# Kernel tuning notes

Hardware: AMD Instinct MI355X
Metric: run time of the kernel (lower is better)

The kernel has to match this reference:

```python
import jax, jax.numpy as jnp
import numpy as np

N = 100000   # nodes
E = 1600000  # edges
IN, H, C = 128, 128, 64
LN_EPS = 1e-5


def _xavier(key, fan_in, fan_out):
    lim = jnp.sqrt(6.0 / (fan_in + fan_out)).astype(jnp.float32)
    return jax.random.uniform(key, (fan_in, fan_out), jnp.float32, -lim, lim)


def setup_inputs() -> dict:
    key = jax.random.key(0)
    ks = jax.random.split(key, 6)
    feats = jax.random.normal(ks[0], (N, IN), jnp.float32)
    src = jax.random.randint(ks[1], (E,), 0, N, jnp.int32)
    dst = jax.random.randint(ks[2], (E,), 0, N, jnp.int32)
    return {
        "feats": feats, "src": src, "dst": dst,
        "W0": _xavier(ks[3], IN, H), "b0": jnp.zeros((H,), jnp.float32),
        "g0": jnp.ones((H,), jnp.float32), "be0": jnp.zeros((H,), jnp.float32),
        "W1": _xavier(ks[4], H, H), "b1": jnp.zeros((H,), jnp.float32),
        "g1": jnp.ones((H,), jnp.float32), "be1": jnp.zeros((H,), jnp.float32),
        "W2": _xavier(ks[5], H, C), "b2": jnp.zeros((C,), jnp.float32),
    }


def _gcn_agg(h, src, dst):
    # symmetric GCN normalization: out[v] = sum_{(u,v) in E} h[u] / sqrt(deg_out(u) * deg_in(v))
    ones = jnp.ones(src.shape, jnp.float32)
    deg_out = jax.ops.segment_sum(ones, src, num_segments=N)
    deg_in = jax.ops.segment_sum(ones, dst, num_segments=N)
    norm_o = jax.lax.rsqrt(jnp.maximum(deg_out, 1.0))
    norm_i = jax.lax.rsqrt(jnp.maximum(deg_in, 1.0))
    msg = (h * norm_o[:, None])[src]                       # [E, d] gather
    agg = jax.ops.segment_sum(msg, dst, num_segments=N)    # [N, d] scatter-add
    return agg * norm_i[:, None]


def _layernorm(x, gamma, beta):
    mu = jnp.mean(x, axis=-1, keepdims=True)
    var = jnp.mean(jnp.square(x - mu), axis=-1, keepdims=True)
    return (x - mu) * jax.lax.rsqrt(var + LN_EPS) * gamma + beta


def reference(feats, src, dst, W0, b0, g0, be0, W1, b1, g1, be1, W2, b2):
    # layer 0: agg -> matmul -> bias -> dropout(eval: identity) -> layernorm -> relu
    h = _gcn_agg(feats, src, dst) @ W0 + b0
    h = jax.nn.relu(_layernorm(h, g0, be0))
    # layer 1
    h = _gcn_agg(h, src, dst) @ W1 + b1
    h = jax.nn.relu(_layernorm(h, g1, be1))
    # final layer: agg -> matmul -> bias
    out = _gcn_agg(h, src, dst) @ W2 + b2
    return out
```

## Files before the change

### kernel.cpp

```cpp
#include <hip/hip_runtime.h>

constexpr float LN_EPS = 1e-5f;

typedef __bf16 bf16x8 __attribute__((ext_vector_type(8)));
typedef float f32x4 __attribute__((ext_vector_type(4)));

__device__ __forceinline__ unsigned short f2bf(float f) {
  unsigned int u = __float_as_uint(f);
  u = (u + 0x7fffu + ((u >> 16) & 1u)) >> 16;
  return (unsigned short)u;
}
__device__ __forceinline__ float bflo(unsigned int p) { return __uint_as_float(p << 16); }
__device__ __forceinline__ float bfhi(unsigned int p) { return __uint_as_float(p & 0xffff0000u); }

#define NPB 256
#define CHUNK 4096

__global__ __launch_bounds__(256) void passA_kernel(
    const int* __restrict__ src, const int* __restrict__ dst,
    int* __restrict__ cntD, int* __restrict__ cntS, int NB, int NBLK, int E) {
  extern __shared__ int sh[];
  for (int j = threadIdx.x; j < 2 * NB; j += 256) sh[j] = 0;
  __syncthreads();
  const int blk = blockIdx.x;
  const int base = blk * CHUNK;
  const int end = min(base + CHUNK, E);
  for (int i = base + threadIdx.x; i < end; i += 256) {
    atomicAdd(&sh[dst[i] >> 8], 1);
    atomicAdd(&sh[NB + (src[i] >> 8)], 1);
  }
  __syncthreads();
  for (int j = threadIdx.x; j < NB; j += 256) {
    cntD[j * NBLK + blk] = sh[j];
    cntS[j * NBLK + blk] = sh[NB + j];
  }
}

__global__ __launch_bounds__(512) void scan1_kernel(
    const int* __restrict__ cntD, const int* __restrict__ cntS,
    int* __restrict__ offLD, int* __restrict__ offLS,
    int* __restrict__ totD, int* __restrict__ totS, int NB, int NBLK) {
  __shared__ int p[512];
  const int t = threadIdx.x;
  const bool isS = blockIdx.x >= NB;
  const int b = isS ? blockIdx.x - NB : blockIdx.x;
  const int* cnt = isS ? cntS : cntD;
  int* offL = isS ? offLS : offLD;
  int own = (t < NBLK) ? cnt[b * NBLK + t] : 0;
  p[t] = own;
  __syncthreads();
  for (int off = 1; off < 512; off <<= 1) {
    int x = (t >= off) ? p[t - off] : 0;
    __syncthreads();
    p[t] += x;
    __syncthreads();
  }
  if (t < NBLK) offL[b * NBLK + t] = p[t] - own;
  if (t == 511) (isS ? totS : totD)[b] = p[511];
}

__global__ __launch_bounds__(512) void scan2_kernel(
    const int* __restrict__ totD, const int* __restrict__ totS,
    int* __restrict__ bktD, int* __restrict__ bktS,
    int* __restrict__ row_st, int NB, int N, int E) {
  __shared__ int p[512];
  const int t = threadIdx.x;
  int own = (t < NB) ? totD[t] : 0;
  p[t] = own;
  __syncthreads();
  for (int off = 1; off < 512; off <<= 1) {
    int x = (t >= off) ? p[t - off] : 0;
    __syncthreads();
    p[t] += x;
    __syncthreads();
  }
  if (t < NB) bktD[t] = p[t] - own;
  __syncthreads();
  int own2 = (t < NB) ? totS[t] : 0;
  p[t] = own2;
  __syncthreads();
  for (int off = 1; off < 512; off <<= 1) {
    int x = (t >= off) ? p[t - off] : 0;
    __syncthreads();
    p[t] += x;
    __syncthreads();
  }
  if (t < NB) bktS[t] = p[t] - own2;
  if (t == 0) {
    bktD[NB] = E;
    bktS[NB] = E;
    row_st[N] = E;
  }
}

__global__ __launch_bounds__(256) void passB_kernel(
    const int* __restrict__ src, const int* __restrict__ dst,
    const int* __restrict__ offLD, const int* __restrict__ offLS,
    const int* __restrict__ bkt_stD, const int* __restrict__ bkt_stS,
    unsigned int* __restrict__ packedD, unsigned char* __restrict__ srcS,
    int NB, int NBLK, int E) {
  __shared__ unsigned int sD[CHUNK];
  __shared__ unsigned short bD_[CHUNK];
  __shared__ unsigned char sS_[CHUNK];
  __shared__ unsigned short bS_[CHUNK];
  __shared__ int hD[512], lD[512], hS[512], lS[512];
  const int t = threadIdx.x;
  const int blk = blockIdx.x;
  const int base = blk * CHUNK;
  const int end = min(base + CHUNK, E);
  const int cnt = end - base;
  hD[t] = 0; hD[t + 256] = 0; hS[t] = 0; hS[t + 256] = 0;
  __syncthreads();
  for (int i = base + t; i < end; i += 256) {
    atomicAdd(&hD[dst[i] >> 8], 1);
    atomicAdd(&hS[src[i] >> 8], 1);
  }
  __syncthreads();
  int oD0 = hD[t], oD1 = hD[t + 256], oS0 = hS[t], oS1 = hS[t + 256];
  for (int off = 1; off < 512; off <<= 1) {
    int xd0 = (t >= off) ? hD[t - off] : 0;
    int xd1 = (t + 256 >= off) ? hD[t + 256 - off] : 0;
    int xs0 = (t >= off) ? hS[t - off] : 0;
    int xs1 = (t + 256 >= off) ? hS[t + 256 - off] : 0;
    __syncthreads();
    hD[t] += xd0; hD[t + 256] += xd1;
    hS[t] += xs0; hS[t + 256] += xs1;
    __syncthreads();
  }
  lD[t] = hD[t] - oD0; lD[t + 256] = hD[t + 256] - oD1;
  lS[t] = hS[t] - oS0; lS[t + 256] = hS[t + 256] - oS1;
  __syncthreads();
  hD[t] = lD[t]; hD[t + 256] = lD[t + 256];
  hS[t] = lS[t]; hS[t + 256] = lS[t + 256];
  __syncthreads();
  for (int i = base + t; i < end; i += 256) {
    const int d = dst[i];
    const int s = src[i];
    const int bD = d >> 8;
    const int pD = atomicAdd(&hD[bD], 1);
    sD[pD] = ((unsigned int)(d & 255) << 24) | (unsigned int)s;
    bD_[pD] = (unsigned short)bD;
    const int bS = s >> 8;
    const int pS = atomicAdd(&hS[bS], 1);
    sS_[pS] = (unsigned char)(s & 255);
    bS_[pS] = (unsigned short)bS;
  }
  __syncthreads();
  for (int i = t; i < cnt; i += 256) {
    const int bD = bD_[i];
    packedD[bkt_stD[bD] + offLD[bD * NBLK + blk] + (i - lD[bD])] = sD[i];
    const int bS = bS_[i];
    srcS[bkt_stS[bS] + offLS[bS * NBLK + blk] + (i - lS[bS])] = sS_[i];
  }
}

__global__ __launch_bounds__(256) void passC_kernel(
    const unsigned int* __restrict__ packed, const int* __restrict__ bucket_start,
    int* __restrict__ row_st, float* __restrict__ ni,
    int* __restrict__ edge_src, int N) {
  __shared__ int cnt[NPB];
  __shared__ int cur[NPB];
  __shared__ int tmp[NPB];
  const int b = blockIdx.x;
  const int t = threadIdx.x;
  const int v0 = b * NPB;
  const int bs = bucket_start[b];
  const int be = bucket_start[b + 1];
  cnt[t] = 0;
  __syncthreads();
  for (int i = bs + t; i < be; i += 256)
    atomicAdd(&cnt[packed[i] >> 24], 1);
  __syncthreads();
  int own = cnt[t];
  tmp[t] = own;
  __syncthreads();
  for (int off = 1; off < NPB; off <<= 1) {
    int x = (t >= off) ? tmp[t - off] : 0;
    __syncthreads();
    tmp[t] += x;
    __syncthreads();
  }
  const int pref = tmp[t] - own;
  if (v0 + t < N) {
    row_st[v0 + t] = bs + pref;
    ni[v0 + t] = rsqrtf(fmaxf((float)own, 1.0f));
  }
  cur[t] = bs + pref;
  __syncthreads();
  for (int i = bs + t; i < be; i += 256) {
    unsigned int p = packed[i];
    int pos = atomicAdd(&cur[p >> 24], 1);
    edge_src[pos] = (int)(p & 0xFFFFFFu);
  }
}

__global__ __launch_bounds__(256) void passD_kernel(
    const unsigned char* __restrict__ srcS, const int* __restrict__ bkt_stS,
    float* __restrict__ no, int N) {
  __shared__ int cnt[NPB];
  const int b = blockIdx.x;
  const int t = threadIdx.x;
  cnt[t] = 0;
  __syncthreads();
  const int bs = bkt_stS[b];
  const int be = bkt_stS[b + 1];
  for (int i = bs + t; i < be; i += 256)
    atomicAdd(&cnt[srcS[i]], 1);
  __syncthreads();
  const int v = b * NPB + t;
  if (v < N) no[v] = rsqrtf(fmaxf((float)cnt[t], 1.0f));
}

__global__ void wconv_kernel(const float* __restrict__ W, unsigned short* __restrict__ Wt,
                             int K, int C) {
  int i = blockIdx.x * blockDim.x + threadIdx.x;
  if (i < K * C) {
    int k = i / C, c = i - k * C;
    Wt[c * K + k] = f2bf(W[i]);
  }
}

__global__ __launch_bounds__(256) void featconv_kernel(const float* __restrict__ F,
                                                       const float* __restrict__ no,
                                                       unsigned short* __restrict__ out, int N) {
  int row = blockIdx.x * 8 + (threadIdx.x >> 5);
  if (row >= N) return;
  int c = (threadIdx.x & 31) * 4;
  float4 v = *reinterpret_cast<const float4*>(F + (size_t)row * 128 + c);
  float nof = no[row];
  unsigned int lo = (unsigned int)f2bf(v.x * nof) | ((unsigned int)f2bf(v.y * nof) << 16);
  unsigned int hi = (unsigned int)f2bf(v.z * nof) | ((unsigned int)f2bf(v.w * nof) << 16);
  uint2 p = {lo, hi};
  *reinterpret_cast<uint2*>(out + (size_t)row * 128 + c) = p;
}

__global__ __launch_bounds__(256) void gather_agg_b(
    const unsigned short* __restrict__ hB, const int* __restrict__ row_start,
    const int* __restrict__ edge_src, const float* __restrict__ ni,
    unsigned short* __restrict__ aggB, int N) {
  const int v = blockIdx.x * 4 + (threadIdx.x >> 6);
  if (v >= N) return;
  const int lane = threadIdx.x & 63;
  const int s = row_start[v];
  const int e = row_start[v + 1];
  float a0 = 0.f, a1 = 0.f, b0 = 0.f, b1 = 0.f;
  float c0 = 0.f, c1 = 0.f, d0 = 0.f, d1 = 0.f;
  int j = s;
  for (; j + 4 <= e; j += 4) {
    int u0 = edge_src[j], u1 = edge_src[j + 1], u2 = edge_src[j + 2], u3 = edge_src[j + 3];
    unsigned int p0 = *reinterpret_cast<const unsigned int*>(hB + (size_t)u0 * 128 + 2 * lane);
    unsigned int p1 = *reinterpret_cast<const unsigned int*>(hB + (size_t)u1 * 128 + 2 * lane);
    unsigned int p2 = *reinterpret_cast<const unsigned int*>(hB + (size_t)u2 * 128 + 2 * lane);
    unsigned int p3 = *reinterpret_cast<const unsigned int*>(hB + (size_t)u3 * 128 + 2 * lane);
    a0 += bflo(p0); a1 += bfhi(p0);
    b0 += bflo(p1); b1 += bfhi(p1);
    c0 += bflo(p2); c1 += bfhi(p2);
    d0 += bflo(p3); d1 += bfhi(p3);
  }
  for (; j < e; ++j) {
    unsigned int p0 = *reinterpret_cast<const unsigned int*>(hB + (size_t)edge_src[j] * 128 + 2 * lane);
    a0 += bflo(p0); a1 += bfhi(p0);
  }
  const float niv = ni[v];
  a0 = ((a0 + b0) + (c0 + d0)) * niv;
  a1 = ((a1 + b1) + (c1 + d1)) * niv;
  unsigned int po = (unsigned int)f2bf(a0) | ((unsigned int)f2bf(a1) << 16);
  *reinterpret_cast<unsigned int*>(aggB + (size_t)v * 128 + 2 * lane) = po;
}

__global__ __launch_bounds__(256) void mm_mfma_ln(
    const unsigned short* __restrict__ A, const unsigned short* __restrict__ Wt,
    const float* __restrict__ b, const float* __restrict__ g,
    const float* __restrict__ be, const float* __restrict__ no,
    unsigned short* __restrict__ out, int N) {
  __shared__ float sS[2][2][16];
  __shared__ float sQ[2][2][16];
  __shared__ float sNo[32];
  const int rbase = blockIdx.x * 32;
  const int w = threadIdx.x >> 6;
  const int l = threadIdx.x & 63;
  const int rt = w & 1, ch = w >> 1;
  if (threadIdx.x < 32) sNo[threadIdx.x] = no[min(rbase + (int)threadIdx.x, N - 1)];
  const int arow = min(rbase + rt * 16 + (l & 15), N - 1);
  const int kof = (l >> 4) * 8;

  bf16x8 af[4];
  const unsigned short* ap = A + (size_t)arow * 128 + kof;
#pragma unroll
  for (int kk = 0; kk < 4; ++kk)
    af[kk] = *reinterpret_cast<const bf16x8*>(ap + kk * 32);

  f32x4 acc[4] = {};
#pragma unroll
  for (int ct = 0; ct < 4; ++ct) {
    const int ccol = ch * 64 + ct * 16 + (l & 15);
    const unsigned short* bp = Wt + (size_t)ccol * 128 + kof;
#pragma unroll
    for (int kk = 0; kk < 4; ++kk) {
      bf16x8 bfr = *reinterpret_cast<const bf16x8*>(bp + kk * 32);
      acc[ct] = __builtin_amdgcn_mfma_f32_16x16x32_bf16(af[kk], bfr, acc[ct], 0, 0, 0);
    }
  }

  float s[4] = {0.f, 0.f, 0.f, 0.f}, q[4] = {0.f, 0.f, 0.f, 0.f};
#pragma unroll
  for (int ct = 0; ct < 4; ++ct) {
    const float bc = b[ch * 64 + ct * 16 + (l & 15)];
#pragma unroll
    for (int j = 0; j < 4; ++j) {
      float v = acc[ct][j] + bc;
      acc[ct][j] = v;
      s[j] += v;
      q[j] += v * v;
    }
  }
#pragma unroll
  for (int j = 0; j < 4; ++j) {
#pragma unroll
    for (int off = 1; off < 16; off <<= 1) {
      s[j] += __shfl_xor(s[j], off);
      q[j] += __shfl_xor(q[j], off);
    }
  }
  const int grp = l >> 4;
  if ((l & 15) == 0) {
#pragma unroll
    for (int j = 0; j < 4; ++j) {
      sS[rt][ch][grp * 4 + j] = s[j];
      sQ[rt][ch][grp * 4 + j] = q[j];
    }
  }
  __syncthreads();

#pragma unroll
  for (int j = 0; j < 4; ++j) {
    const int r = grp * 4 + j;
    const int row = rbase + rt * 16 + r;
    float S = sS[rt][0][r] + sS[rt][1][r];
    float Q = sQ[rt][0][r] + sQ[rt][1][r];
    float mu = S * (1.f / 128.f);
    float rstd = rsqrtf(fmaxf(Q * (1.f / 128.f) - mu * mu, 0.f) + LN_EPS);
    float nof = sNo[rt * 16 + r];
    if (row < N) {
#pragma unroll
      for (int ct = 0; ct < 4; ++ct) {
        const int ccol = ch * 64 + ct * 16 + (l & 15);
        float y = (acc[ct][j] - mu) * rstd * g[ccol] + be[ccol];
        y = fmaxf(y, 0.f) * nof;
        out[(size_t)row * 128 + ccol] = f2bf(y);
      }
    }
  }
}

__global__ __launch_bounds__(256) void mm_final_mfma(
    const unsigned short* __restrict__ A, const unsigned short* __restrict__ Wt,
    const float* __restrict__ b, float* __restrict__ out, int N) {
  const int rbase = blockIdx.x * 32;
  const int w = threadIdx.x >> 6;
  const int l = threadIdx.x & 63;
  const int rt = w & 1, ch = w >> 1;
  const int arow = min(rbase + rt * 16 + (l & 15), N - 1);
  const int kof = (l >> 4) * 8;

  bf16x8 af[4];
  const unsigned short* ap = A + (size_t)arow * 128 + kof;
#pragma unroll
  for (int kk = 0; kk < 4; ++kk)
    af[kk] = *reinterpret_cast<const bf16x8*>(ap + kk * 32);

  f32x4 acc[2] = {};
#pragma unroll
  for (int ct = 0; ct < 2; ++ct) {
    const int ccol = ch * 32 + ct * 16 + (l & 15);
    const unsigned short* bp = Wt + (size_t)ccol * 128 + kof;
#pragma unroll
    for (int kk = 0; kk < 4; ++kk) {
      bf16x8 bfr = *reinterpret_cast<const bf16x8*>(bp + kk * 32);
      acc[ct] = __builtin_amdgcn_mfma_f32_16x16x32_bf16(af[kk], bfr, acc[ct], 0, 0, 0);
    }
  }
  const int grp = l >> 4;
#pragma unroll
  for (int ct = 0; ct < 2; ++ct) {
    const int ccol = ch * 32 + ct * 16 + (l & 15);
    const float bc = b[ccol];
#pragma unroll
    for (int j = 0; j < 4; ++j) {
      const int row = rbase + rt * 16 + grp * 4 + j;
      if (row < N) out[(size_t)row * 64 + ccol] = acc[ct][j] + bc;
    }
  }
}

extern "C" void kernel_launch(void* const* d_in, const int* in_sizes, int n_in,
                              void* d_out, int out_size, void* d_ws, size_t ws_size,
                              hipStream_t stream) {
  const float* feats = (const float*)d_in[0];
  const int*   src   = (const int*)d_in[1];
  const int*   dst   = (const int*)d_in[2];
  const float* W0    = (const float*)d_in[3];
  const float* b0    = (const float*)d_in[4];
  const float* g0    = (const float*)d_in[5];
  const float* be0   = (const float*)d_in[6];
  const float* W1    = (const float*)d_in[7];
  const float* b1    = (const float*)d_in[8];
  const float* g1    = (const float*)d_in[9];
  const float* be1   = (const float*)d_in[10];
  const float* W2    = (const float*)d_in[11];
  const float* b2    = (const float*)d_in[12];
  float* out = (float*)d_out;

  const int n = in_sizes[0] / 128;
  const int e = in_sizes[1];
  const int NB = (n + NPB - 1) / NPB;
  const int NBLK = (e + CHUNK - 1) / CHUNK;

  float* ws = (float*)d_ws;
  auto pad4 = [](size_t x) { return (x + 3) & ~(size_t)3; };
  size_t o = 0;
  float* norm_o  = ws + o; o = pad4(o + n);
  float* norm_i  = ws + o; o = pad4(o + n);
  int*   cntD    = (int*)(ws + o); o = pad4(o + (size_t)NB * NBLK);
  int*   cntS    = (int*)(ws + o); o = pad4(o + (size_t)NB * NBLK);
  int*   offLD   = (int*)(ws + o); o = pad4(o + (size_t)NB * NBLK);
  int*   offLS   = (int*)(ws + o); o = pad4(o + (size_t)NB * NBLK);
  int*   totD    = (int*)(ws + o); o = pad4(o + NB);
  int*   totS    = (int*)(ws + o); o = pad4(o + NB);
  int*   bkt_stD = (int*)(ws + o); o = pad4(o + NB + 1);
  int*   bkt_stS = (int*)(ws + o); o = pad4(o + NB + 1);
  int*   row_st  = (int*)(ws + o); o = pad4(o + n + 1);
  unsigned int*  packedD = (unsigned int*)(ws + o);  o = pad4(o + (size_t)e);
  unsigned char* srcS    = (unsigned char*)(ws + o); o = pad4(o + (size_t)(e + 3) / 4);
  int*   edg_src = (int*)(ws + o); o = pad4(o + (size_t)e);
  unsigned short* featB = (unsigned short*)(ws + o); o = pad4(o + (size_t)n * 64);
  unsigned short* aggB  = (unsigned short*)(ws + o); o = pad4(o + (size_t)n * 64);
  unsigned short* Wt0   = (unsigned short*)(ws + o); o = pad4(o + 128 * 128 / 2);
  unsigned short* Wt1   = (unsigned short*)(ws + o); o = pad4(o + 128 * 128 / 2);
  unsigned short* Wt2   = (unsigned short*)(ws + o); o = pad4(o + 128 * 64 / 2);
  unsigned short* hB = featB;

  passA_kernel<<<NBLK, 256, 2 * NB * sizeof(int), stream>>>(src, dst, cntD, cntS, NB, NBLK, e);
  scan1_kernel<<<2 * NB, 512, 0, stream>>>(cntD, cntS, offLD, offLS, totD, totS, NB, NBLK);
  scan2_kernel<<<1, 512, 0, stream>>>(totD, totS, bkt_stD, bkt_stS, row_st, NB, n, e);
  passB_kernel<<<NBLK, 256, 0, stream>>>(src, dst, offLD, offLS, bkt_stD, bkt_stS,
                                         packedD, srcS, NB, NBLK, e);
  passC_kernel<<<NB, 256, 0, stream>>>(packedD, bkt_stD, row_st, norm_i, edg_src, n);
  passD_kernel<<<NB, 256, 0, stream>>>(srcS, bkt_stS, norm_o, n);

  wconv_kernel<<<(128 * 128 + 255) / 256, 256, 0, stream>>>(W0, Wt0, 128, 128);
  wconv_kernel<<<(128 * 128 + 255) / 256, 256, 0, stream>>>(W1, Wt1, 128, 128);
  wconv_kernel<<<(128 * 64 + 255) / 256, 256, 0, stream>>>(W2, Wt2, 128, 64);
  featconv_kernel<<<(n + 7) / 8, 256, 0, stream>>>(feats, norm_o, featB, n);

  const int gblocks = (n + 3) / 4;
  const int mblocks = (n + 31) / 32;

  gather_agg_b<<<gblocks, 256, 0, stream>>>(featB, row_st, edg_src, norm_i, aggB, n);
  mm_mfma_ln<<<mblocks, 256, 0, stream>>>(aggB, Wt0, b0, g0, be0, norm_o, hB, n);
  gather_agg_b<<<gblocks, 256, 0, stream>>>(hB, row_st, edg_src, norm_i, aggB, n);
  mm_mfma_ln<<<mblocks, 256, 0, stream>>>(aggB, Wt1, b1, g1, be1, norm_o, hB, n);
  gather_agg_b<<<gblocks, 256, 0, stream>>>(hB, row_st, edg_src, norm_i, aggB, n);
  mm_final_mfma<<<mblocks, 256, 0, stream>>>(aggB, Wt2, b2, out, n);
}
```

Baseline: 431.5 us.

## Reorder final layer to matmul before aggregation and widen gather loads

The final layer now multiplies by W2 first (128->64) and then aggregates the 64-wide bf16 result, with the bias added after aggregation. This halves the gather traffic for the last layer, relying on aggregation being linear. Separately, the gather kernels split each wavefront into two halves that process alternate edges using 8-byte loads, combined with a cross-half shuffle. The extra bf16 rounding of the pre-aggregation product slightly changes numerics.

```diff
diff --git a/kernel.cpp b/kernel.cpp
--- a/kernel.cpp
+++ b/kernel.cpp
@@ -9,6 +9,9 @@
   unsigned int u = __float_as_uint(f);
   u = (u + 0x7fffu + ((u >> 16) & 1u)) >> 16;
   return (unsigned short)u;
+}
+__device__ __forceinline__ unsigned int pk2(float x, float y) {
+  return (unsigned int)f2bf(x) | ((unsigned int)f2bf(y) << 16);
 }
 __device__ __forceinline__ float bflo(unsigned int p) { return __uint_as_float(p << 16); }
 __device__ __forceinline__ float bfhi(unsigned int p) { return __uint_as_float(p & 0xffff0000u); }
@@ -228,9 +231,7 @@
   int c = (threadIdx.x & 31) * 4;
   float4 v = *reinterpret_cast<const float4*>(F + (size_t)row * 128 + c);
   float nof = no[row];
-  unsigned int lo = (unsigned int)f2bf(v.x * nof) | ((unsigned int)f2bf(v.y * nof) << 16);
-  unsigned int hi = (unsigned int)f2bf(v.z * nof) | ((unsigned int)f2bf(v.w * nof) << 16);
-  uint2 p = {lo, hi};
+  uint2 p = {pk2(v.x * nof, v.y * nof), pk2(v.z * nof, v.w * nof)};
   *reinterpret_cast<uint2*>(out + (size_t)row * 128 + c) = p;
 }
 
@@ -240,32 +241,104 @@
     unsigned short* __restrict__ aggB, int N) {
   const int v = blockIdx.x * 4 + (threadIdx.x >> 6);
   if (v >= N) return;
-  const int lane = threadIdx.x & 63;
+  const int l = threadIdx.x & 63;
+  const int half = l >> 5;
+  const int lane = l & 31;
   const int s = row_start[v];
   const int e = row_start[v + 1];
-  float a0 = 0.f, a1 = 0.f, b0 = 0.f, b1 = 0.f;
-  float c0 = 0.f, c1 = 0.f, d0 = 0.f, d1 = 0.f;
+  const int co = 4 * lane;
+  float a0 = 0, a1 = 0, a2 = 0, a3 = 0;
+  float b0 = 0, b1 = 0, b2 = 0, b3 = 0;
+  float c0 = 0, c1 = 0, c2 = 0, c3 = 0;
+  float d0 = 0, d1 = 0, d2 = 0, d3 = 0;
   int j = s;
-  for (; j + 4 <= e; j += 4) {
-    int u0 = edge_src[j], u1 = edge_src[j + 1], u2 = edge_src[j + 2], u3 = edge_src[j + 3];
-    unsigned int p0 = *reinterpret_cast<const unsigned int*>(hB + (size_t)u0 * 128 + 2 * lane);
-    unsigned int p1 = *reinterpret_cast<const unsigned int*>(hB + (size_t)u1 * 128 + 2 * lane);
-    unsigned int p2 = *reinterpret_cast<const unsigned int*>(hB + (size_t)u2 * 128 + 2 * lane);
-    unsigned int p3 = *reinterpret_cast<const unsigned int*>(hB + (size_t)u3 * 128 + 2 * lane);
+  for (; j + 8 <= e; j += 8) {
+    int u0 = edge_src[j + half];
+    int u1 = edge_src[j + 2 + half];
+    int u2 = edge_src[j + 4 + half];
+    int u3 = edge_src[j + 6 + half];
+    uint2 p0 = *reinterpret_cast<const uint2*>(hB + (size_t)u0 * 128 + co);
+    uint2 p1 = *reinterpret_cast<const uint2*>(hB + (size_t)u1 * 128 + co);
+    uint2 p2 = *reinterpret_cast<const uint2*>(hB + (size_t)u2 * 128 + co);
+    uint2 p3 = *reinterpret_cast<const uint2*>(hB + (size_t)u3 * 128 + co);
+    a0 += bflo(p0.x); a1 += bfhi(p0.x); a2 += bflo(p0.y); a3 += bfhi(p0.y);
+    b0 += bflo(p1.x); b1 += bfhi(p1.x); b2 += bflo(p1.y); b3 += bfhi(p1.y);
+    c0 += bflo(p2.x); c1 += bfhi(p2.x); c2 += bflo(p2.y); c3 += bfhi(p2.y);
+    d0 += bflo(p3.x); d1 += bfhi(p3.x); d2 += bflo(p3.y); d3 += bfhi(p3.y);
+  }
+  for (; j + 2 <= e; j += 2) {
+    int u0 = edge_src[j + half];
+    uint2 p0 = *reinterpret_cast<const uint2*>(hB + (size_t)u0 * 128 + co);
+    a0 += bflo(p0.x); a1 += bfhi(p0.x); a2 += bflo(p0.y); a3 += bfhi(p0.y);
+  }
+  if (j < e && half == 0) {
+    int u0 = edge_src[j];
+    uint2 p0 = *reinterpret_cast<const uint2*>(hB + (size_t)u0 * 128 + co);
+    a0 += bflo(p0.x); a1 += bfhi(p0.x); a2 += bflo(p0.y); a3 += bfhi(p0.y);
+  }
+  a0 = (a0 + b0) + (c0 + d0);
+  a1 = (a1 + b1) + (c1 + d1);
+  a2 = (a2 + b2) + (c2 + d2);
+  a3 = (a3 + b3) + (c3 + d3);
+  a0 += __shfl_xor(a0, 32);
+  a1 += __shfl_xor(a1, 32);
+  a2 += __shfl_xor(a2, 32);
+  a3 += __shfl_xor(a3, 32);
+  if (half == 0) {
+    const float niv = ni[v];
+    uint2 po = {pk2(a0 * niv, a1 * niv), pk2(a2 * niv, a3 * niv)};
+    *reinterpret_cast<uint2*>(aggB + (size_t)v * 128 + co) = po;
+  }
+}
+
+__global__ __launch_bounds__(256) void gather_out(
+    const unsigned short* __restrict__ zB, const int* __restrict__ row_start,
+    const int* __restrict__ edge_src, const float* __restrict__ ni,
+    const float* __restrict__ bias, float* __restrict__ out, int N) {
+  const int v = blockIdx.x * 4 + (threadIdx.x >> 6);
+  if (v >= N) return;
+  const int l = threadIdx.x & 63;
+  const int half = l >> 5;
+  const int lane = l & 31;
+  const int s = row_start[v];
+  const int e = row_start[v + 1];
+  const int co = 2 * lane;
+  float a0 = 0, a1 = 0, b0 = 0, b1 = 0, c0 = 0, c1 = 0, d0 = 0, d1 = 0;
+  int j = s;
+  for (; j + 8 <= e; j += 8) {
+    int u0 = edge_src[j + half];
+    int u1 = edge_src[j + 2 + half];
+    int u2 = edge_src[j + 4 + half];
+    int u3 = edge_src[j + 6 + half];
+    unsigned int p0 = *reinterpret_cast<const unsigned int*>(zB + (size_t)u0 * 64 + co);
+    unsigned int p1 = *reinterpret_cast<const unsigned int*>(zB + (size_t)u1 * 64 + co);
+    unsigned int p2 = *reinterpret_cast<const unsigned int*>(zB + (size_t)u2 * 64 + co);
+    unsigned int p3 = *reinterpret_cast<const unsigned int*>(zB + (size_t)u3 * 64 + co);
     a0 += bflo(p0); a1 += bfhi(p0);
     b0 += bflo(p1); b1 += bfhi(p1);
     c0 += bflo(p2); c1 += bfhi(p2);
     d0 += bflo(p3); d1 += bfhi(p3);
   }
-  for (; j < e; ++j) {
-    unsigned int p0 = *reinterpret_cast<const unsigned int*>(hB + (size_t)edge_src[j] * 128 + 2 * lane);
+  for (; j + 2 <= e; j += 2) {
+    int u0 = edge_src[j + half];
+    unsigned int p0 = *reinterpret_cast<const unsigned int*>(zB + (size_t)u0 * 64 + co);
     a0 += bflo(p0); a1 += bfhi(p0);
   }
-  const float niv = ni[v];
-  a0 = ((a0 + b0) + (c0 + d0)) * niv;
-  a1 = ((a1 + b1) + (c1 + d1)) * niv;
-  unsigned int po = (unsigned int)f2bf(a0) | ((unsigned int)f2bf(a1) << 16);
-  *reinterpret_cast<unsigned int*>(aggB + (size_t)v * 128 + 2 * lane) = po;
+  if (j < e && half == 0) {
+    int u0 = edge_src[j];
+    unsigned int p0 = *reinterpret_cast<const unsigned int*>(zB + (size_t)u0 * 64 + co);
+    a0 += bflo(p0); a1 += bfhi(p0);
+  }
+  a0 = (a0 + b0) + (c0 + d0);
+  a1 = (a1 + b1) + (c1 + d1);
+  a0 += __shfl_xor(a0, 32);
+  a1 += __shfl_xor(a1, 32);
+  if (half == 0) {
+    const float niv = ni[v];
+    float2 bb = *reinterpret_cast<const float2*>(bias + co);
+    float2 w = {a0 * niv + bb.x, a1 * niv + bb.y};
+    *reinterpret_cast<float2*>(out + (size_t)v * 64 + co) = w;
+  }
 }
 
 __global__ __launch_bounds__(256) void mm_mfma_ln(
@@ -353,9 +426,9 @@
   }
 }
 
-__global__ __launch_bounds__(256) void mm_final_mfma(
+__global__ __launch_bounds__(256) void mm_z_mfma(
     const unsigned short* __restrict__ A, const unsigned short* __restrict__ Wt,
-    const float* __restrict__ b, float* __restrict__ out, int N) {
+    unsigned short* __restrict__ zB, int N) {
   const int rbase = blockIdx.x * 32;
   const int w = threadIdx.x >> 6;
   const int l = threadIdx.x & 63;
@@ -384,11 +457,10 @@
 #pragma unroll
   for (int ct = 0; ct < 2; ++ct) {
     const int ccol = ch * 32 + ct * 16 + (l & 15);
-    const float bc = b[ccol];
 #pragma unroll
     for (int j = 0; j < 4; ++j) {
       const int row = rbase + rt * 16 + grp * 4 + j;
-      if (row < N) out[(size_t)row * 64 + ccol] = acc[ct][j] + bc;
+      if (row < N) zB[(size_t)row * 64 + ccol] = f2bf(acc[ct][j]);
     }
   }
 }
@@ -439,6 +511,7 @@
   unsigned short* Wt1   = (unsigned short*)(ws + o); o = pad4(o + 128 * 128 / 2);
   unsigned short* Wt2   = (unsigned short*)(ws + o); o = pad4(o + 128 * 64 / 2);
   unsigned short* hB = featB;
+  unsigned short* zB = aggB;
 
   passA_kernel<<<NBLK, 256, 2 * NB * sizeof(int), stream>>>(src, dst, cntD, cntS, NB, NBLK, e);
   scan1_kernel<<<2 * NB, 512, 0, stream>>>(cntD, cntS, offLD, offLS, totD, totS, NB, NBLK);
@@ -460,6 +533,6 @@
   mm_mfma_ln<<<mblocks, 256, 0, stream>>>(aggB, Wt0, b0, g0, be0, norm_o, hB, n);
   gather_agg_b<<<gblocks, 256, 0, stream>>>(hB, row_st, edg_src, norm_i, aggB, n);
   mm_mfma_ln<<<mblocks, 256, 0, stream>>>(aggB, Wt1, b1, g1, be1, norm_o, hB, n);
-  gather_agg_b<<<gblocks, 256, 0, stream>>>(hB, row_st, edg_src, norm_i, aggB, n);
-  mm_final_mfma<<<mblocks, 256, 0, stream>>>(aggB, Wt2, b2, out, n);
-}
+  mm_z_mfma<<<mblocks, 256, 0, stream>>>(hB, Wt2, zB, n);
+  gather_out<<<gblocks, 256, 0, stream>>>(zB, row_st, edg_src, norm_i, b2, out, n);
+}
```

Result: faster. 397.3 us (-7.9%).
